# Kernel optimization log

Hardware: AMD Instinct MI355X
Metric: run time of the kernel (lower is better)

Reference implementation:

```python
import jax, jax.numpy as jnp
import numpy as np

PRUNE_RATIO = 0.5
MIXUP_ALPHA = 0.05


def setup_inputs() -> dict:
    key = jax.random.key(0)
    k1, k2 = jax.random.split(key)
    seq = jax.random.normal(k1, (16, 4096, 1024), dtype=jnp.float32)
    attn_weights = jax.random.normal(k2, (16, 4096), dtype=jnp.float32)
    return {"seq": seq, "attn_weights": attn_weights}


def reference(seq, attn_weights):
    # Eval-mode forward (adversarial_mix only fires in training mode).
    B, N, D = seq.shape
    k = max(1, int(N * (1.0 - PRUNE_RATIO)))  # number of kept tokens
    _, top_idx = jax.lax.top_k(attn_weights, k)  # (B, k) int32
    # gather selected tokens: (B, k, D)
    selected = jnp.take_along_axis(seq, top_idx[:, :, None], axis=1)
    # mask of pruned (non-selected) tokens: ones scattered to zero at top_idx
    batch_ids = jnp.arange(B)[:, None]
    mask = jnp.ones((B, N), dtype=seq.dtype).at[batch_ids, top_idx].set(0.0)
    # masked mean of pruned tokens, scaled by mixup_alpha -> one extra token
    rem_sum = jnp.einsum('bn,bnd->bd', mask, seq)              # (B, D)
    rem_cnt = jnp.sum(mask, axis=1, keepdims=True) + 1e-10     # (B, 1)
    rem_tok = (MIXUP_ALPHA * rem_sum / rem_cnt)[:, None, :]    # (B, 1, D)
    return jnp.concatenate([selected, rem_tok], axis=1)         # (B, k+1, D)
```

## Files before the change

### kernel.cpp

```cpp
#include <hip/hip_runtime.h>

#define BATCH 16
#define NTOK  4096
#define DIM   1024
#define KSEL  2048
#define NPRUNE 2048
#define SUM_CHUNKS 32
#define ROWS_PER_CHUNK 64

__global__ __launch_bounds__(1024) void topk_sort_kernel(
    const float* __restrict__ w, int* __restrict__ sel, int* __restrict__ pr) {
  __shared__ float v[NTOK];
  __shared__ int   ix[NTOK];
  const int b = blockIdx.x;
  const float* wb = w + (size_t)b * NTOK;
  for (int i = threadIdx.x; i < NTOK; i += 1024) { v[i] = wb[i]; ix[i] = i; }
  __syncthreads();

  for (int k = 2; k <= NTOK; k <<= 1) {
    for (int j = k >> 1; j > 0; j >>= 1) {
      for (int i = threadIdx.x; i < NTOK; i += 1024) {
        const int p = i ^ j;
        if (p > i) {
          const float vi = v[i], vp = v[p];
          const int   ii = ix[i], ip = ix[p];
          const bool before = (vi > vp) || (vi == vp && ii < ip);
          const bool up = ((i & k) == 0);
          if (up ? !before : before) {
            v[i] = vp; v[p] = vi; ix[i] = ip; ix[p] = ii;
          }
        }
      }
      __syncthreads();
    }
  }

  for (int i = threadIdx.x; i < KSEL; i += 1024)   sel[b * KSEL + i]   = ix[i];
  for (int i = threadIdx.x; i < NPRUNE; i += 1024) pr[b * NPRUNE + i]  = ix[KSEL + i];
}

__global__ __launch_bounds__(256) void gather_partial_kernel(
    const float* __restrict__ seq, const int* __restrict__ sel,
    const int* __restrict__ pr, float* __restrict__ out,
    float* __restrict__ part) {
  const int b = blockIdx.y;
  const int t = blockIdx.x;
  const float4* seqb = (const float4*)(seq + (size_t)b * NTOK * DIM);

  if (t < KSEL) {
    const int row = sel[b * KSEL + t];
    const float4* src = seqb + (size_t)row * (DIM / 4);
    float4* dst = (float4*)(out + (size_t)b * (KSEL + 1) * DIM + (size_t)t * DIM);
    dst[threadIdx.x] = src[threadIdx.x];
  } else {
    const int c = t - KSEL;
    const int* prb = pr + b * NPRUNE + c * ROWS_PER_CHUNK;
    float4 acc = make_float4(0.f, 0.f, 0.f, 0.f);
    for (int r = 0; r < ROWS_PER_CHUNK; ++r) {
      const int row = prb[r];
      const float4 x = seqb[(size_t)row * (DIM / 4) + threadIdx.x];
      acc.x += x.x; acc.y += x.y; acc.z += x.z; acc.w += x.w;
    }
    float4* pdst = (float4*)(part + ((size_t)b * SUM_CHUNKS + c) * DIM);
    pdst[threadIdx.x] = acc;
  }
}

__global__ __launch_bounds__(256) void reduce_kernel(
    const float* __restrict__ part, float* __restrict__ out, float scale) {
  const int b = blockIdx.x;
  const float4* p = (const float4*)(part + (size_t)b * SUM_CHUNKS * DIM);
  float4 acc = make_float4(0.f, 0.f, 0.f, 0.f);
  for (int c = 0; c < SUM_CHUNKS; ++c) {
    const float4 x = p[(size_t)c * (DIM / 4) + threadIdx.x];
    acc.x += x.x; acc.y += x.y; acc.z += x.z; acc.w += x.w;
  }
  float4* dst = (float4*)(out + (size_t)b * (KSEL + 1) * DIM + (size_t)KSEL * DIM);
  float4 r;
  r.x = acc.x * scale; r.y = acc.y * scale;
  r.z = acc.z * scale; r.w = acc.w * scale;
  dst[threadIdx.x] = r;
}

extern "C" void kernel_launch(void* const* d_in, const int* in_sizes, int n_in,
                              void* d_out, int out_size, void* d_ws, size_t ws_size,
                              hipStream_t stream) {
  (void)in_sizes; (void)n_in; (void)out_size; (void)ws_size;
  const float* seq = (const float*)d_in[0];
  const float* w   = (const float*)d_in[1];
  float* out = (float*)d_out;

  int* sel = (int*)d_ws;
  int* pr  = sel + BATCH * KSEL;
  float* part = (float*)(pr + BATCH * NPRUNE);

  topk_sort_kernel<<<BATCH, 1024, 0, stream>>>(w, sel, pr);
  gather_partial_kernel<<<dim3(KSEL + SUM_CHUNKS, BATCH), 256, 0, stream>>>(
      seq, sel, pr, out, part);
  const float scale = (float)(0.05 / (2048.0 + 1e-10));
  reduce_kernel<<<BATCH, 256, 0, stream>>>(part, out, scale);
}
```

Baseline: 467.6 us.

## Replace bitonic top-k sort with parallel rank counting and batch gather rows

Swaps the per-batch single-block bitonic sort for a rank kernel. Each thread computes its token's rank by comparing a packed 64-bit key (order-flipped float bits plus index) against all 4096 keys held in shared memory, spread over 16x16 blocks. The goal is to remove a serial, sync-heavy sort that runs on only 16 blocks. The gather kernel now copies 4 rows per block and puts the pruned-row sum on 64 chunks with 4 independent accumulators, to raise memory-level parallelism. The rank approach does O(N^2) comparisons per batch, but these are spread over many blocks.

```diff
diff --git a/kernel.cpp b/kernel.cpp
--- a/kernel.cpp
+++ b/kernel.cpp
@@ -5,38 +5,36 @@
 #define DIM   1024
 #define KSEL  2048
 #define NPRUNE 2048
-#define SUM_CHUNKS 32
-#define ROWS_PER_CHUNK 64
+#define SLICES (NTOK / 256)
+#define SUM_CHUNKS 64
+#define ROWS_PER_CHUNK (NPRUNE / SUM_CHUNKS)
+#define COPY_ROWS 4
+#define NCOPY (KSEL / COPY_ROWS)
 
-__global__ __launch_bounds__(1024) void topk_sort_kernel(
+__global__ __launch_bounds__(256) void rank_kernel(
     const float* __restrict__ w, int* __restrict__ sel, int* __restrict__ pr) {
-  __shared__ float v[NTOK];
-  __shared__ int   ix[NTOK];
-  const int b = blockIdx.x;
+  __shared__ unsigned long long keys[NTOK];
+  const int b = blockIdx.y;
   const float* wb = w + (size_t)b * NTOK;
-  for (int i = threadIdx.x; i < NTOK; i += 1024) { v[i] = wb[i]; ix[i] = i; }
+  for (int j = threadIdx.x; j < NTOK; j += 256) {
+    const unsigned int u = __float_as_uint(wb[j]);
+    const unsigned int s = (u & 0x80000000u) ? ~u : (u | 0x80000000u);
+    keys[j] = ((unsigned long long)(~s) << 32) | (unsigned int)j;
+  }
   __syncthreads();
 
-  for (int k = 2; k <= NTOK; k <<= 1) {
-    for (int j = k >> 1; j > 0; j >>= 1) {
-      for (int i = threadIdx.x; i < NTOK; i += 1024) {
-        const int p = i ^ j;
-        if (p > i) {
-          const float vi = v[i], vp = v[p];
-          const int   ii = ix[i], ip = ix[p];
-          const bool before = (vi > vp) || (vi == vp && ii < ip);
-          const bool up = ((i & k) == 0);
-          if (up ? !before : before) {
-            v[i] = vp; v[p] = vi; ix[i] = ip; ix[p] = ii;
-          }
-        }
-      }
-      __syncthreads();
-    }
+  const int i = blockIdx.x * 256 + threadIdx.x;
+  const unsigned long long ki = keys[i];
+  const ulonglong2* k2 = (const ulonglong2*)keys;
+  unsigned int rank = 0;
+#pragma unroll 8
+  for (int j = 0; j < NTOK / 2; ++j) {
+    const ulonglong2 kk = k2[j];
+    rank += (kk.x < ki);
+    rank += (kk.y < ki);
   }
-
-  for (int i = threadIdx.x; i < KSEL; i += 1024)   sel[b * KSEL + i]   = ix[i];
-  for (int i = threadIdx.x; i < NPRUNE; i += 1024) pr[b * NPRUNE + i]  = ix[KSEL + i];
+  if (rank < KSEL) sel[b * KSEL + rank] = i;
+  else             pr[b * NPRUNE + (rank - KSEL)] = i;
 }
 
 __global__ __launch_bounds__(256) void gather_partial_kernel(
@@ -46,23 +44,45 @@
   const int b = blockIdx.y;
   const int t = blockIdx.x;
   const float4* seqb = (const float4*)(seq + (size_t)b * NTOK * DIM);
+  const int lane = threadIdx.x;
 
-  if (t < KSEL) {
-    const int row = sel[b * KSEL + t];
-    const float4* src = seqb + (size_t)row * (DIM / 4);
-    float4* dst = (float4*)(out + (size_t)b * (KSEL + 1) * DIM + (size_t)t * DIM);
-    dst[threadIdx.x] = src[threadIdx.x];
+  if (t < SUM_CHUNKS) {
+    const int* prb = pr + b * NPRUNE + t * ROWS_PER_CHUNK;
+    float4 a0 = make_float4(0.f, 0.f, 0.f, 0.f), a1 = a0, a2 = a0, a3 = a0;
+    for (int r = 0; r < ROWS_PER_CHUNK; r += 4) {
+      const int r0 = prb[r + 0], r1 = prb[r + 1];
+      const int r2 = prb[r + 2], r3 = prb[r + 3];
+      const float4 x0 = seqb[(size_t)r0 * (DIM / 4) + lane];
+      const float4 x1 = seqb[(size_t)r1 * (DIM / 4) + lane];
+      const float4 x2 = seqb[(size_t)r2 * (DIM / 4) + lane];
+      const float4 x3 = seqb[(size_t)r3 * (DIM / 4) + lane];
+      a0.x += x0.x; a0.y += x0.y; a0.z += x0.z; a0.w += x0.w;
+      a1.x += x1.x; a1.y += x1.y; a1.z += x1.z; a1.w += x1.w;
+      a2.x += x2.x; a2.y += x2.y; a2.z += x2.z; a2.w += x2.w;
+      a3.x += x3.x; a3.y += x3.y; a3.z += x3.z; a3.w += x3.w;
+    }
+    float4 acc;
+    acc.x = (a0.x + a1.x) + (a2.x + a3.x);
+    acc.y = (a0.y + a1.y) + (a2.y + a3.y);
+    acc.z = (a0.z + a1.z) + (a2.z + a3.z);
+    acc.w = (a0.w + a1.w) + (a2.w + a3.w);
+    float4* pdst = (float4*)(part + ((size_t)b * SUM_CHUNKS + t) * DIM);
+    pdst[lane] = acc;
   } else {
-    const int c = t - KSEL;
-    const int* prb = pr + b * NPRUNE + c * ROWS_PER_CHUNK;
-    float4 acc = make_float4(0.f, 0.f, 0.f, 0.f);
-    for (int r = 0; r < ROWS_PER_CHUNK; ++r) {
-      const int row = prb[r];
-      const float4 x = seqb[(size_t)row * (DIM / 4) + threadIdx.x];
-      acc.x += x.x; acc.y += x.y; acc.z += x.z; acc.w += x.w;
-    }
-    float4* pdst = (float4*)(part + ((size_t)b * SUM_CHUNKS + c) * DIM);
-    pdst[threadIdx.x] = acc;
+    const int c = t - SUM_CHUNKS;
+    const int base = c * COPY_ROWS;
+    const int* selb = sel + b * KSEL + base;
+    const int i0 = selb[0], i1 = selb[1], i2 = selb[2], i3 = selb[3];
+    const float4 x0 = seqb[(size_t)i0 * (DIM / 4) + lane];
+    const float4 x1 = seqb[(size_t)i1 * (DIM / 4) + lane];
+    const float4 x2 = seqb[(size_t)i2 * (DIM / 4) + lane];
+    const float4 x3 = seqb[(size_t)i3 * (DIM / 4) + lane];
+    float4* dst = (float4*)(out + (size_t)b * (KSEL + 1) * DIM +
+                            (size_t)base * DIM);
+    dst[0 * (DIM / 4) + lane] = x0;
+    dst[1 * (DIM / 4) + lane] = x1;
+    dst[2 * (DIM / 4) + lane] = x2;
+    dst[3 * (DIM / 4) + lane] = x3;
   }
 }
 
@@ -75,7 +95,8 @@
     const float4 x = p[(size_t)c * (DIM / 4) + threadIdx.x];
     acc.x += x.x; acc.y += x.y; acc.z += x.z; acc.w += x.w;
   }
-  float4* dst = (float4*)(out + (size_t)b * (KSEL + 1) * DIM + (size_t)KSEL * DIM);
+  float4* dst = (float4*)(out + (size_t)b * (KSEL + 1) * DIM +
+                          (size_t)KSEL * DIM);
   float4 r;
   r.x = acc.x * scale; r.y = acc.y * scale;
   r.z = acc.z * scale; r.w = acc.w * scale;
@@ -94,8 +115,8 @@
   int* pr  = sel + BATCH * KSEL;
   float* part = (float*)(pr + BATCH * NPRUNE);
 
-  topk_sort_kernel<<<BATCH, 1024, 0, stream>>>(w, sel, pr);
-  gather_partial_kernel<<<dim3(KSEL + SUM_CHUNKS, BATCH), 256, 0, stream>>>(
+  rank_kernel<<<dim3(SLICES, BATCH), 256, 0, stream>>>(w, sel, pr);
+  gather_partial_kernel<<<dim3(SUM_CHUNKS + NCOPY, BATCH), 256, 0, stream>>>(
       seq, sel, pr, out, part);
   const float scale = (float)(0.05 / (2048.0 + 1e-10));
   reduce_kernel<<<BATCH, 256, 0, stream>>>(part, out, scale);
```

After: 453.4 us. 3.0% less time.
